# Kernel optimization log

Hardware: AMD Instinct MI355X
Metric: run time of the kernel (lower is better)

Reference implementation:

```python
import jax, jax.numpy as jnp
import numpy as np

B, N, C = 8, 16384, 4
NUM_GROUPS = 512   # K for farthest point sampling
GROUP_SIZE = 32    # K after energy-based top-k
UPSCALE_K = 512    # ball-query candidate count
RADIUS = 0.5       # group_radius
CONTEXT = 256      # context_length


def _fps_idx(xyz, lengths, K):
    """Iterative farthest point sampling. xyz: (B,P,3). Returns (B,K) int32 indices.
    Start point is index 0 (random_start_point=False). Assumes lengths >= K."""
    Bn, P, _ = xyz.shape
    valid = jnp.arange(P)[None, :] < lengths[:, None]
    start = jnp.zeros((Bn,), jnp.int32)
    mind0 = jnp.full((Bn, P), jnp.float32(1e10))

    def step(carry, _):
        mind, last = carry
        lastpt = jnp.take_along_axis(xyz, last[:, None, None], axis=1)  # (B,1,3)
        d = jnp.sum((xyz - lastpt) ** 2, axis=-1)                       # (B,P)
        mind = jnp.minimum(mind, d)
        nxt = jnp.argmax(jnp.where(valid, mind, -jnp.inf), axis=1).astype(jnp.int32)
        return (mind, nxt), nxt

    _, rest = jax.lax.scan(step, (mind0, start), None, length=K - 1)  # (K-1,B)
    return jnp.concatenate([start[:, None], rest.T], axis=1)          # (B,K)


def _masked_gather(points, idx):
    """torch masked_gather: -1 indices are replaced with 0 before gathering."""
    idx0 = jnp.maximum(idx, 0)
    if idx.ndim == 3:
        Bn, G, K = idx.shape
        out = jnp.take_along_axis(points, idx0.reshape(Bn, G * K)[:, :, None], axis=1)
        return out.reshape(Bn, G, K, points.shape[-1])
    return jnp.take_along_axis(points, idx0[:, :, None], axis=1)


def _ball_query(centers, xyz, lengths, K, radius):
    """First-K points within radius of each center, in original index order; pad -1."""
    P = xyz.shape[1]
    d2 = jnp.sum((centers[:, :, None, :] - xyz[:, None, :, :]) ** 2, axis=-1)  # (B,G,P)
    valid = (d2 < radius * radius) & (jnp.arange(P)[None, None, :] < lengths[:, None, None])
    # key = -index for valid points, -P for invalid -> top_k gives first valid indices
    key = jnp.where(valid, -jnp.arange(P, dtype=jnp.int32)[None, None, :], jnp.int32(-P))
    vals, pos = jax.lax.top_k(key, K)           # (B,G,K)
    return jnp.where(vals > -P, pos, -1)


def _topk_by_energy(points, idx, K):
    """Keep the K highest-energy (channel 3) points per group; pad -1."""
    Bn, G, Ko = idx.shape
    e = points[..., 3]                                                  # (B,P)
    eb = jnp.broadcast_to(e[:, None, :], (Bn, G, e.shape[1]))
    energies = jnp.take_along_axis(eb, jnp.maximum(idx, 0), axis=2)     # (B,G,Ko)
    energies = jnp.where(idx == -1, -jnp.inf, energies)
    top_e, top_pos = jax.lax.top_k(energies, K)
    top_idx = jnp.take_along_axis(idx, top_pos, axis=2)
    return jnp.where(jnp.isneginf(top_e), -1, top_idx)


def setup_inputs() -> dict:
    key = jax.random.key(0)
    k1, k2 = jax.random.split(key)
    points = jax.random.normal(k1, (B, N, C), dtype=jnp.float32)
    lengths = jax.random.randint(k2, (B,), 3 * N // 4, N + 1, dtype=jnp.int32)
    return {"points": points, "lengths": lengths}


def reference(points, lengths):
    # FPS -> group centers (kept with all C channels, as in masked_gather(points, idx))
    centers_idx = _fps_idx(points[:, :, :3], lengths, NUM_GROUPS)
    group_centers = _masked_gather(points, centers_idx)                 # (B,G,C)
    # Ball query around centers
    idx = _ball_query(group_centers[:, :, :3], points[:, :, :3], lengths, UPSCALE_K, RADIUS)
    # Energy-based reduction to GROUP_SIZE points per group
    idx = _topk_by_energy(points, idx, GROUP_SIZE)                      # (B,G,Ks)
    point_lengths = jnp.sum(idx != -1, axis=2)                          # (B,G)
    # fill_empty_indices: replace -1 with the group's first index
    filled = jnp.where(idx == -1, idx[:, :, :1], idx)
    groups = _masked_gather(points, filled)                             # (B,G,Ks,C)
    point_mask = jnp.arange(GROUP_SIZE)[None, None, :] < point_lengths[:, :CONTEXT, None]
    G = idx.shape[1]
    group_lengths = jnp.sum(jnp.all(idx != -1, axis=2), axis=1)         # (B,)
    embedding_mask = jnp.arange(G)[None, :] < group_lengths[:, None]
    return (groups[:, :CONTEXT], group_centers[:, :CONTEXT],
            embedding_mask[:, :CONTEXT], point_mask)
```

## Files before the change

kernel.cpp:

```cpp
#include <hip/hip_runtime.h>
#include <stdint.h>

#define NB   8
#define NP   16384
#define NG   512
#define GS   32
#define UPK  512
#define CTX  256

#define OFF_CENTERS (NB*CTX*GS*4)
#define OFF_EMB     (OFF_CENTERS + NB*CTX*4)
#define OFF_PMASK   (OFF_EMB + NB*CTX)

typedef unsigned long long u64;
typedef unsigned int u32;

#define SENT 0xFFFFFFFFFFFFFFFFull
#define PUB  32
#define NWK  31

__device__ __forceinline__ u32 fkey(float f) {
  union { float f; u32 u; } v; v.f = f;
  u32 s = v.u;
  return s ^ ((s & 0x80000000u) ? 0xFFFFFFFFu : 0x80000000u);
}

__device__ __forceinline__ float dist2(float ax, float ay, float az,
                                       float bx, float by, float bz) {
  float dx = __fsub_rn(ax, bx);
  float dy = __fsub_rn(ay, by);
  float dz = __fsub_rn(az, bz);
  return __fadd_rn(__fadd_rn(__fmul_rn(dx, dx), __fmul_rn(dy, dy)),
                   __fmul_rn(dz, dz));
}

template<int CTRL, int RM>
__device__ __forceinline__ u64 dpp_max_u64(u64 k) {
  int lo = (int)(u32)k, hi = (int)(u32)(k >> 32);
  int mlo = __builtin_amdgcn_update_dpp(lo, lo, CTRL, RM, 0xf, false);
  int mhi = __builtin_amdgcn_update_dpp(hi, hi, CTRL, RM, 0xf, false);
  u64 o = ((u64)(u32)mhi << 32) | (u32)mlo;
  return o > k ? o : k;
}

__device__ __forceinline__ u64 wave_max_u64(u64 k) {
  k = dpp_max_u64<0x111, 0xf>(k);
  k = dpp_max_u64<0x112, 0xf>(k);
  k = dpp_max_u64<0x114, 0xf>(k);
  k = dpp_max_u64<0x118, 0xf>(k);
  k = dpp_max_u64<0x142, 0xa>(k);
  k = dpp_max_u64<0x143, 0xc>(k);
  return k;
}

__device__ __forceinline__ u64 read_lane_u64(u64 k, int lane) {
  u32 lo = (u32)__builtin_amdgcn_readlane((int)(u32)k, lane);
  u32 hi = (u32)__builtin_amdgcn_readlane((int)(u32)(k >> 32), lane);
  return ((u64)hi << 32) | lo;
}

struct FpsSmem {
  u64 sred[2][8];
  int s_centers[NG];
};
struct WkSmem {
  u64 masks[256];
  u32 scnt[256];
  u32 spre[256];
  u32 swsum[8];
  float candE[UPK];
  int   candI[UPK];
  int   s_T, s_pl;
  int   s_win[GS];
  u64   s_cc[2];
};
union SmemU { FpsSmem f; WkSmem w; };
struct Smem { SmemU u; char pad[81920]; };

__device__ __forceinline__ void publish_center(u64* __restrict__ cb,
                                               float* __restrict__ out,
                                               int b, int w, float4 q) {
  u64 lo = ((u64)__float_as_uint(q.y) << 32) | __float_as_uint(q.x);
  u64 hi = ((u64)__float_as_uint(q.w) << 32) | __float_as_uint(q.z);
  __hip_atomic_store(&cb[2 * w],     lo, __ATOMIC_RELAXED, __HIP_MEMORY_SCOPE_AGENT);
  __hip_atomic_store(&cb[2 * w + 1], hi, __ATOMIC_RELAXED, __HIP_MEMORY_SCOPE_AGENT);
  if (w < CTX) ((float4*)(out + OFF_CENTERS))[b * CTX + w] = q;
}

#define FPS_T 512
#define PPT   (NP / FPS_T)

__global__ __launch_bounds__(FPS_T)
__attribute__((amdgpu_waves_per_eu(2, 2)))
void fused_kernel(const float4* __restrict__ pts, const int* __restrict__ lengths,
                  u64* __restrict__ cws, int* __restrict__ group_len,
                  float* __restrict__ out)
{
  __shared__ Smem sm;
  const int blk  = blockIdx.x;
  const int tid  = threadIdx.x;
  const int lane = tid & 63;
  const int wave = tid >> 6;

  if (blk < NB) {
    FpsSmem& F = sm.u.f;
    const int b = blk;
    const float4* p = pts + (size_t)b * NP;
    const int len = lengths[b];
    u64* cb = cws + (size_t)b * NG * 2;

    const float4 q0 = p[0];
    float px[PPT], py[PPT], pz[PPT], mind[PPT];
#pragma unroll
    for (int j = 0; j < PPT; j++) {
      int i = tid + j * FPS_T;
      float4 q = p[i];
      if (i >= len) q = q0;
      px[j] = q.x; py[j] = q.y; pz[j] = q.z;
      mind[j] = 1e10f;
    }
    if (tid == 0) F.s_centers[0] = 0;

    int last = 0;
    for (int it = 1; it < NG; it++) {
      float4 lp = p[last];
      float tmax = -1.0f; int tj = 0;
#pragma unroll
      for (int j = 0; j < PPT; j++) {
        float d = dist2(px[j], py[j], pz[j], lp.x, lp.y, lp.z);
        float m = fminf(mind[j], d);
        mind[j] = m;
        bool c = m > tmax;
        tmax = c ? m : tmax;
        tj   = c ? j : tj;
      }
      int gidx = tid + (tj << 9);
      u64 key = ((u64)__float_as_uint(tmax) << 32) | (u32)(~gidx);
      key = wave_max_u64(key);
      u64 wkey = read_lane_u64(key, 63);
      if (lane == 0) F.sred[it & 1][wave] = wkey;
      __syncthreads();
      u64 k2 = F.sred[it & 1][lane & 7];
      k2 = dpp_max_u64<0x111, 0xf>(k2);
      k2 = dpp_max_u64<0x112, 0xf>(k2);
      k2 = dpp_max_u64<0x114, 0xf>(k2);
      u64 bk = read_lane_u64(k2, 7);
      last = (int)(~(u32)bk) & (NP - 1);
      if (tid == 0) F.s_centers[it] = last;
      if ((it & (PUB - 1)) == 0 && tid < PUB) {
        int w = it - PUB + tid;
        int ci = F.s_centers[w] & (NP - 1);
        publish_center(cb, out, b, w, p[ci]);
      }
    }
    __syncthreads();
    if (tid < PUB) {
      int w = NG - PUB + tid;
      int ci = F.s_centers[w] & (NP - 1);
      publish_center(cb, out, b, w, p[ci]);
    }
    return;
  }

  WkSmem& S = sm.u.w;
  const int b  = blk & (NB - 1);
  const int wi = (blk >> 3) - 1;
  const float4* p = pts + (size_t)b * NP;
  const int len = lengths[b];
  u64* cb = cws + (size_t)b * NG * 2;

  for (int g = wi; g < NG; g += NWK) {
    if (tid == 0) {
      u64 lo, hi;
      while ((lo = __hip_atomic_load(&cb[2 * g], __ATOMIC_RELAXED,
                                     __HIP_MEMORY_SCOPE_AGENT)) == SENT)
        __builtin_amdgcn_s_sleep(8);
      while ((hi = __hip_atomic_load(&cb[2 * g + 1], __ATOMIC_RELAXED,
                                     __HIP_MEMORY_SCOPE_AGENT)) == SENT)
        __builtin_amdgcn_s_sleep(1);
      S.s_cc[0] = lo; S.s_cc[1] = hi;
    }
    __syncthreads();
    const float cx = __uint_as_float((u32)S.s_cc[0]);
    const float cy = __uint_as_float((u32)(S.s_cc[0] >> 32));
    const float cz = __uint_as_float((u32)S.s_cc[1]);

    if (g >= CTX) {
      u32 c = 0;
      for (int step = 0; step < 32; step++) {
        int i = step * 512 + tid;
        if (i < len) {
          float4 q = p[i];
          float d = dist2(cx, cy, cz, q.x, q.y, q.z);
          c += (d < 0.25f) ? 1u : 0u;
        }
      }
#pragma unroll
      for (int off = 32; off; off >>= 1) c += __shfl_down(c, (unsigned)off, 64);
      if (lane == 0) S.swsum[wave] = c;
      __syncthreads();
      if (tid == 0) {
        u32 total = 0;
#pragma unroll
        for (int w = 0; w < 8; w++) total += S.swsum[w];
        if (total >= GS) atomicAdd(&group_len[b], 1);
      }
      __syncthreads();
      continue;
    }

    for (int step = 0; step < 32; step++) {
      int i = step * 512 + tid;
      bool flag = false;
      if (i < len) {
        float4 q = p[i];
        float d = dist2(cx, cy, cz, q.x, q.y, q.z);
        flag = d < 0.25f;
      }
      u64 m = __ballot(flag);
      if (lane == 0) S.masks[step * 8 + wave] = m;
    }
    __syncthreads();

    u32 cnt = 0, sc = 0;
    if (tid < 256) {
      cnt = (u32)__popcll(S.masks[tid]);
      sc = cnt;
#pragma unroll
      for (int off = 1; off < 64; off <<= 1) {
        u32 o = __shfl_up(sc, (unsigned)off, 64);
        if (lane >= off) sc += o;
      }
      if (lane == 63) S.swsum[wave] = sc;
    }
    __syncthreads();
    const u32 total = S.swsum[0] + S.swsum[1] + S.swsum[2] + S.swsum[3];
    if (tid < 256) {
      u32 woff = 0;
#pragma unroll
      for (int w = 0; w < 4; w++) woff += (w < wave) ? S.swsum[w] : 0u;
      u32 incl = sc + woff;
      S.scnt[tid] = cnt;
      S.spre[tid] = incl;
      if (total > UPK) {
        u32 ex = incl - cnt;
        if (ex <= (UPK - 1) && incl > (UPK - 1)) {
          u32 r = (UPK - 1) - ex;
          u64 m = S.masks[tid];
          for (u32 k = 0; k < r; k++) m &= m - 1;
          S.s_T = tid * 64 + ((int)__ffsll((unsigned long long)m) - 1);
        }
      } else if (tid == 0) S.s_T = NP - 1;
    }
    __syncthreads();
    const int T = S.s_T;

    for (int step = 0; step < 32; step++) {
      int i  = step * 512 + tid;
      int ch = step * 8 + wave;
      u64 m = S.masks[ch];
      if (((m >> lane) & 1ull) && i <= T) {
        u32 pos = ((S.spre[ch] - S.scnt[ch]) +
                   (u32)__popcll(m & ((1ull << lane) - 1ull))) & (UPK - 1);
        S.candE[pos] = ((const float*)p)[i * 4 + 3];
        S.candI[pos] = i;
      }
    }
    __syncthreads();

    const int ncand = (int)(total < UPK ? total : UPK);

    if (wave == 0) {
      u64 k[8];
#pragma unroll
      for (int t = 0; t < 8; t++) {
        int ci = lane + t * 64;
        k[t] = (ci < ncand) ? (((u64)fkey(S.candE[ci]) << 32) | (u32)(~ci)) : 0ull;
      }
      int pl = 0;
      for (int r = 0; r < GS; r++) {
        u64 bm = k[0];
#pragma unroll
        for (int t = 1; t < 8; t++) if (k[t] > bm) bm = k[t];
#pragma unroll
        for (int off = 32; off; off >>= 1) {
          u64 o = __shfl_xor(bm, (unsigned)off, 64);
          if (o > bm) bm = o;
        }
        if (bm == 0) break;
        int pos = (int)(~(u32)bm) & (UPK - 1);
        if (lane == 0) S.s_win[r] = S.candI[pos];
        int ol = pos & 63, ot = pos >> 6;
#pragma unroll
        for (int t = 0; t < 8; t++)
          if (t == ot && lane == ol) k[t] = 0;
        pl = r + 1;
      }
      if (lane == 0) {
        int f0 = (pl > 0) ? S.s_win[0] : 0;
        for (int r = pl; r < GS; r++) S.s_win[r] = f0;
        S.s_pl = pl;
      }
    }
    __syncthreads();

    const int base = b * CTX + g;
    if (tid < GS) {
      int fi = S.s_win[tid] & (NP - 1);
      float4 q = p[fi];
      ((float4*)out)[base * GS + tid] = q;
      out[OFF_PMASK + base * GS + tid] = (tid < S.s_pl) ? 1.0f : 0.0f;
    }
    if (tid == 0 && total >= GS) atomicAdd(&group_len[b], 1);
    __syncthreads();
  }
}

__global__ void init_kernel(u64* __restrict__ cws, int* __restrict__ group_len)
{
  int i = blockIdx.x * blockDim.x + threadIdx.x;
  if (i < NB * NG * 2)
    __hip_atomic_store(&cws[i], SENT, __ATOMIC_RELAXED, __HIP_MEMORY_SCOPE_AGENT);
  if (i < NB) group_len[i] = 0;
}

__global__ void emb_kernel(const int* __restrict__ group_len,
                           float* __restrict__ out)
{
  int i = blockIdx.x * blockDim.x + threadIdx.x;
  if (i < NB * CTX) {
    int b = i >> 8;
    int g = i & 255;
    out[OFF_EMB + i] = (g < group_len[b]) ? 1.0f : 0.0f;
  }
}

extern "C" void kernel_launch(void* const* d_in, const int* in_sizes, int n_in,
                              void* d_out, int out_size, void* d_ws, size_t ws_size,
                              hipStream_t stream)
{
  const float4* pts     = (const float4*)d_in[0];
  const int*    lengths = (const int*)d_in[1];
  float* out = (float*)d_out;

  u64* cws       = (u64*)d_ws;
  int* group_len = (int*)((char*)d_ws + (size_t)NB * NG * sizeof(float4));

  init_kernel<<<(NB * NG * 2 + 255) / 256, 256, 0, stream>>>(cws, group_len);
  fused_kernel<<<NB + NB * NWK, FPS_T, 0, stream>>>(pts, lengths, cws, group_len, out);
  emb_kernel<<<(NB * CTX + 255) / 256, 256, 0, stream>>>(group_len, out);
}
```

Measured before the change: 707.1 us.

## Publish FPS center indices per iteration and fold embedding mask into worker

The FPS block now stores each selected center index into the workspace with an atomic store on every iteration, replacing the batched 32-center publication of full coordinates. Worker blocks read the index and gather the center from the points themselves, which lets them start earlier. The count-only path for groups beyond the context length now counts with a ballot popcount and stops once GS hits are found. The separate embedding-mask kernel is removed: the last worker block per batch, found through an atomic completion counter, writes the mask. In exchange there is one extra dependent global load per group, and the last-block handoff relies on acquire/release ordering being correct.

```diff
diff --git a/kernel.cpp b/kernel.cpp
--- a/kernel.cpp
+++ b/kernel.cpp
@@ -15,9 +15,8 @@
 typedef unsigned long long u64;
 typedef unsigned int u32;
 
-#define SENT 0xFFFFFFFFFFFFFFFFull
-#define PUB  32
-#define NWK  31
+#define SENT32 0xFFFFFFFFu
+#define NWK    31
 
 __device__ __forceinline__ u32 fkey(float f) {
   union { float f; u32 u; } v; v.f = f;
@@ -61,7 +60,6 @@
 
 struct FpsSmem {
   u64 sred[2][8];
-  int s_centers[NG];
 };
 struct WkSmem {
   u64 masks[256];
@@ -71,30 +69,21 @@
   float candE[UPK];
   int   candI[UPK];
   int   s_T, s_pl;
+  int   s_fin, s_gl;
   int   s_win[GS];
-  u64   s_cc[2];
+  float4 s_cc;
 };
 union SmemU { FpsSmem f; WkSmem w; };
 struct Smem { SmemU u; char pad[81920]; };
 
-__device__ __forceinline__ void publish_center(u64* __restrict__ cb,
-                                               float* __restrict__ out,
-                                               int b, int w, float4 q) {
-  u64 lo = ((u64)__float_as_uint(q.y) << 32) | __float_as_uint(q.x);
-  u64 hi = ((u64)__float_as_uint(q.w) << 32) | __float_as_uint(q.z);
-  __hip_atomic_store(&cb[2 * w],     lo, __ATOMIC_RELAXED, __HIP_MEMORY_SCOPE_AGENT);
-  __hip_atomic_store(&cb[2 * w + 1], hi, __ATOMIC_RELAXED, __HIP_MEMORY_SCOPE_AGENT);
-  if (w < CTX) ((float4*)(out + OFF_CENTERS))[b * CTX + w] = q;
-}
-
 #define FPS_T 512
 #define PPT   (NP / FPS_T)
 
 __global__ __launch_bounds__(FPS_T)
 __attribute__((amdgpu_waves_per_eu(2, 2)))
 void fused_kernel(const float4* __restrict__ pts, const int* __restrict__ lengths,
-                  u64* __restrict__ cws, int* __restrict__ group_len,
-                  float* __restrict__ out)
+                  u32* __restrict__ cws, int* __restrict__ group_len,
+                  int* __restrict__ wdone, float* __restrict__ out)
 {
   __shared__ Smem sm;
   const int blk  = blockIdx.x;
@@ -107,7 +96,9 @@
     const int b = blk;
     const float4* p = pts + (size_t)b * NP;
     const int len = lengths[b];
-    u64* cb = cws + (size_t)b * NG * 2;
+    u32* cb = cws + (size_t)b * NG;
+    if (tid == 0)
+      __hip_atomic_store(&cb[0], 0u, __ATOMIC_RELAXED, __HIP_MEMORY_SCOPE_AGENT);
 
     const float4 q0 = p[0];
     float px[PPT], py[PPT], pz[PPT], mind[PPT];
@@ -119,7 +110,6 @@
       px[j] = q.x; py[j] = q.y; pz[j] = q.z;
       mind[j] = 1e10f;
     }
-    if (tid == 0) F.s_centers[0] = 0;
 
     int last = 0;
     for (int it = 1; it < NG; it++) {
@@ -146,18 +136,9 @@
       k2 = dpp_max_u64<0x114, 0xf>(k2);
       u64 bk = read_lane_u64(k2, 7);
       last = (int)(~(u32)bk) & (NP - 1);
-      if (tid == 0) F.s_centers[it] = last;
-      if ((it & (PUB - 1)) == 0 && tid < PUB) {
-        int w = it - PUB + tid;
-        int ci = F.s_centers[w] & (NP - 1);
-        publish_center(cb, out, b, w, p[ci]);
-      }
-    }
-    __syncthreads();
-    if (tid < PUB) {
-      int w = NG - PUB + tid;
-      int ci = F.s_centers[w] & (NP - 1);
-      publish_center(cb, out, b, w, p[ci]);
+      if (tid == 0)
+        __hip_atomic_store(&cb[it], (u32)last, __ATOMIC_RELAXED,
+                           __HIP_MEMORY_SCOPE_AGENT);
     }
     return;
   }
@@ -167,36 +148,35 @@
   const int wi = (blk >> 3) - 1;
   const float4* p = pts + (size_t)b * NP;
   const int len = lengths[b];
-  u64* cb = cws + (size_t)b * NG * 2;
+  u32* cb = cws + (size_t)b * NG;
 
   for (int g = wi; g < NG; g += NWK) {
     if (tid == 0) {
-      u64 lo, hi;
-      while ((lo = __hip_atomic_load(&cb[2 * g], __ATOMIC_RELAXED,
-                                     __HIP_MEMORY_SCOPE_AGENT)) == SENT)
+      u32 ci;
+      while ((ci = __hip_atomic_load(&cb[g], __ATOMIC_RELAXED,
+                                     __HIP_MEMORY_SCOPE_AGENT)) == SENT32)
         __builtin_amdgcn_s_sleep(8);
-      while ((hi = __hip_atomic_load(&cb[2 * g + 1], __ATOMIC_RELAXED,
-                                     __HIP_MEMORY_SCOPE_AGENT)) == SENT)
-        __builtin_amdgcn_s_sleep(1);
-      S.s_cc[0] = lo; S.s_cc[1] = hi;
-    }
-    __syncthreads();
-    const float cx = __uint_as_float((u32)S.s_cc[0]);
-    const float cy = __uint_as_float((u32)(S.s_cc[0] >> 32));
-    const float cz = __uint_as_float((u32)S.s_cc[1]);
+      float4 q = p[ci];
+      S.s_cc = q;
+      if (g < CTX)
+        ((float4*)(out + OFF_CENTERS))[b * CTX + g] = q;
+    }
+    __syncthreads();
+    const float cx = S.s_cc.x, cy = S.s_cc.y, cz = S.s_cc.z;
 
     if (g >= CTX) {
       u32 c = 0;
       for (int step = 0; step < 32; step++) {
         int i = step * 512 + tid;
+        bool flag = false;
         if (i < len) {
           float4 q = p[i];
           float d = dist2(cx, cy, cz, q.x, q.y, q.z);
-          c += (d < 0.25f) ? 1u : 0u;
+          flag = d < 0.25f;
         }
-      }
-#pragma unroll
-      for (int off = 32; off; off >>= 1) c += __shfl_down(c, (unsigned)off, 64);
+        c += (u32)__popcll(__ballot(flag));
+        if (c >= GS) break;
+      }
       if (lane == 0) S.swsum[wave] = c;
       __syncthreads();
       if (tid == 0) {
@@ -314,25 +294,27 @@
     if (tid == 0 && total >= GS) atomicAdd(&group_len[b], 1);
     __syncthreads();
   }
-}
-
-__global__ void init_kernel(u64* __restrict__ cws, int* __restrict__ group_len)
+
+  if (tid == 0) {
+    int old = __hip_atomic_fetch_add(&wdone[b], 1, __ATOMIC_ACQ_REL,
+                                     __HIP_MEMORY_SCOPE_AGENT);
+    int fin = (old == NWK - 1) ? 1 : 0;
+    S.s_fin = fin;
+    S.s_gl = fin ? __hip_atomic_load(&group_len[b], __ATOMIC_RELAXED,
+                                     __HIP_MEMORY_SCOPE_AGENT) : 0;
+  }
+  __syncthreads();
+  if (S.s_fin && tid < CTX)
+    out[OFF_EMB + b * CTX + tid] = (tid < S.s_gl) ? 1.0f : 0.0f;
+}
+
+__global__ void init_kernel(u32* __restrict__ cws, int* __restrict__ group_len,
+                            int* __restrict__ wdone)
 {
   int i = blockIdx.x * blockDim.x + threadIdx.x;
-  if (i < NB * NG * 2)
-    __hip_atomic_store(&cws[i], SENT, __ATOMIC_RELAXED, __HIP_MEMORY_SCOPE_AGENT);
-  if (i < NB) group_len[i] = 0;
-}
-
-__global__ void emb_kernel(const int* __restrict__ group_len,
-                           float* __restrict__ out)
-{
-  int i = blockIdx.x * blockDim.x + threadIdx.x;
-  if (i < NB * CTX) {
-    int b = i >> 8;
-    int g = i & 255;
-    out[OFF_EMB + i] = (g < group_len[b]) ? 1.0f : 0.0f;
-  }
+  if (i < NB * NG)
+    __hip_atomic_store(&cws[i], SENT32, __ATOMIC_RELAXED, __HIP_MEMORY_SCOPE_AGENT);
+  if (i < NB) { group_len[i] = 0; wdone[i] = 0; }
 }
 
 extern "C" void kernel_launch(void* const* d_in, const int* in_sizes, int n_in,
@@ -343,10 +325,11 @@
   const int*    lengths = (const int*)d_in[1];
   float* out = (float*)d_out;
 
-  u64* cws       = (u64*)d_ws;
-  int* group_len = (int*)((char*)d_ws + (size_t)NB * NG * sizeof(float4));
-
-  init_kernel<<<(NB * NG * 2 + 255) / 256, 256, 0, stream>>>(cws, group_len);
-  fused_kernel<<<NB + NB * NWK, FPS_T, 0, stream>>>(pts, lengths, cws, group_len, out);
-  emb_kernel<<<(NB * CTX + 255) / 256, 256, 0, stream>>>(group_len, out);
-}
+  u32* cws       = (u32*)d_ws;
+  int* group_len = (int*)(cws + NB * NG);
+  int* wdone     = group_len + NB;
+
+  init_kernel<<<(NB * NG + 255) / 256, 256, 0, stream>>>(cws, group_len, wdone);
+  fused_kernel<<<NB + NB * NWK, FPS_T, 0, stream>>>(pts, lengths, cws, group_len,
+                                                    wdone, out);
+}
```

New measurement: 682.6 us, median of 2. -3.5%, faster.
